# Optimization experiments

Hardware: AMD Instinct MI355X
Metric: run time of the kernel (lower is better)

## Reference

```python
import jax, jax.numpy as jnp
import numpy as np

SCALE = 8.0  # sqrt(head_dim=64); module divides scores by self.scale


def setup_inputs() -> dict:
    key = jax.random.key(0)
    kq, kk, kv = jax.random.split(key, 3)
    B, H, L, D = 4, 8, 2048, 64
    queries = jax.random.normal(kq, (B, H, L, D), dtype=jnp.float32)
    keys = jax.random.normal(kk, (B, H, L, D), dtype=jnp.float32)
    values = jax.random.normal(kv, (B, H, L, D), dtype=jnp.float32)
    return {"queries": queries, "keys": keys, "values": values}


def reference(queries, keys, values):
    # scores: [B, H, L_Q, L_K]
    L_Q, L_K = queries.shape[2], keys.shape[2]
    scores = jnp.einsum('bnqd,bnkd->bnqk', queries, keys) / SCALE
    # causal mask: triu(ones, diagonal=1) positions set to -inf
    causal = jnp.triu(jnp.ones((L_Q, L_K), dtype=bool), k=1)
    scores = jnp.where(causal[None, None, :, :], -jnp.inf, scores)
    A = jax.nn.softmax(scores, axis=-1)  # dropout p=0.0 (eval) -> identity
    V = jnp.einsum('bnqk,bnkd->bnqd', A, values)
    return V
```

## Files before the change

### kernel.cpp

```cpp
#include <hip/hip_runtime.h>
#include <hip/hip_bf16.h>

typedef __attribute__((ext_vector_type(8))) short bf16x8;
typedef __attribute__((ext_vector_type(16))) float f32x16;

#define DHEAD 64
#define L_SEQ 2048
#define QSCALE (0.125f * 1.44269504088896340736f)

#define WS_ML_OFF   4096
#define WS_PART_OFF (4096 + 512 * 2 * 128 * 8)
#define WS_NEED     ((size_t)WS_PART_OFF + (size_t)512 * 128 * 64 * 2)

union U4S8 { uint4 u; bf16x8 s; };

__device__ __forceinline__ unsigned pk2(float a, float b) {
    unsigned r;
    asm("v_cvt_pk_bf16_f32 %0, %1, %2" : "=v"(r) : "v"(a), "v"(b));
    return r;
}
__device__ __forceinline__ float bfrt(float x) {
    return __uint_as_float(pk2(x, x) << 16);
}
__device__ __forceinline__ float bf2f(unsigned short u) {
    return __uint_as_float((unsigned)u << 16);
}

__device__ __forceinline__ float fexp2(float x) {
#if __has_builtin(__builtin_amdgcn_exp2f)
    return __builtin_amdgcn_exp2f(x);
#else
    return __expf(x * 0.69314718055994530942f);
#endif
}

#if __has_builtin(__builtin_amdgcn_permlane32_swap)
__device__ __forceinline__ float xhalf_max(float x) {
    const unsigned u = __float_as_uint(x);
    const auto r = __builtin_amdgcn_permlane32_swap(u, u, false, false);
    return fmaxf(__uint_as_float(r[0]), __uint_as_float(r[1]));
}
__device__ __forceinline__ float xhalf_sum(float x) {
    const unsigned u = __float_as_uint(x);
    const auto r = __builtin_amdgcn_permlane32_swap(u, u, false, false);
    return __uint_as_float(r[0]) + __uint_as_float(r[1]);
}
#else
__device__ __forceinline__ float xhalf_max(float x) { return fmaxf(x, __shfl_xor(x, 32)); }
__device__ __forceinline__ float xhalf_sum(float x) { return x + __shfl_xor(x, 32); }
#endif

#define MAX16(P) fmaxf(fmaxf(fmaxf(fmaxf(P[0],P[1]),fmaxf(P[2],P[3])),          \
                             fmaxf(fmaxf(P[4],P[5]),fmaxf(P[6],P[7]))),         \
                       fmaxf(fmaxf(fmaxf(P[8],P[9]),fmaxf(P[10],P[11])),        \
                             fmaxf(fmaxf(P[12],P[13]),fmaxf(P[14],P[15]))))
#define SUM16(P) ((((P[0]+P[1])+(P[2]+P[3]))+((P[4]+P[5])+(P[6]+P[7])))         \
                + (((P[8]+P[9])+(P[10]+P[11]))+((P[12]+P[13])+(P[14]+P[15]))))


template<int SPLIT>
__global__ __launch_bounds__(256, 3)
void fattn_kernel(const float* __restrict__ Qg, const float* __restrict__ Kg,
                  const float* __restrict__ Vg, float* __restrict__ Og,
                  char* __restrict__ wsBase) {
    __shared__ uint4 sK4[16][64];
    __shared__ uint4 sV4[16][64];

    const int tid  = threadIdx.x;
    const int lane = tid & 63;
    const int w    = tid >> 6;
    const int hi   = lane >> 5;
    const int c    = lane & 31;

    const int id  = blockIdx.x;
    const int bh  = (id & 7) + 8 * ((id >> 3) & 3);

    int T, h, kt0, kstep, d;
    if (SPLIT) {
        const int k31 = 31 - (id >> 5);
        T = k31 >> 1;
        h = 1 - (k31 & 1);
        d = (T + 2 - h) >> 1;
        if (d == 0) return;
        kt0 = h; kstep = 2;
    } else {
        const int u_ = id >> 5;
        T = (u_ < 8) ? (15 - u_) : (u_ - 8);
        h = 0; d = T + 1; kt0 = 0; kstep = 1;
    }

    const size_t base = (size_t)bh * L_SEQ * DHEAD;
    const int q0w = T * 128 + w * 32;

    bf16x8 qf[4];
    {
        const float* Qrow = Qg + base + (size_t)(q0w + c) * DHEAD;
        #pragma unroll
        for (int kc = 0; kc < 4; ++kc) {
            float4 aa = *(const float4*)(Qrow + kc * 16 + hi * 8);
            float4 bb = *(const float4*)(Qrow + kc * 16 + hi * 8 + 4);
            U4S8 t;
            t.u = make_uint4(pk2(aa.x * QSCALE, aa.y * QSCALE),
                             pk2(aa.z * QSCALE, aa.w * QSCALE),
                             pk2(bb.x * QSCALE, bb.y * QSCALE),
                             pk2(bb.z * QSCALE, bb.w * QSCALE));
            qf[kc] = t.s;
        }
    }

    const float* Kpb = Kg + base + (size_t)(32 * w + c) * DHEAD + 32 * hi;
    const float* Vpb = Vg + base + (size_t)(32 * w + 16 * hi) * DHEAD + c;

    auto stage_K = [&](int kt) {
        float4 rk[8];
        const float* Kp = Kpb + (size_t)kt * 128 * DHEAD;
        #pragma unroll
        for (int t = 0; t < 8; ++t) rk[t] = *(const float4*)(Kp + 4 * t);
        #pragma unroll
        for (int q = 0; q < 2; ++q)
            #pragma unroll
            for (int hh = 0; hh < 2; ++hh) {
                const float4 r0 = rk[4 * q + 2 * hh], r1 = rk[4 * q + 2 * hh + 1];
                sK4[w * 4 + 2 * hi + q][hh * 32 + c] =
                    make_uint4(pk2(r0.x, r0.y), pk2(r0.z, r0.w),
                               pk2(r1.x, r1.y), pk2(r1.z, r1.w));
            }
    };
    auto stage_V = [&](int kt) {
        float rv[32];
        const float* Vp = Vpb + (size_t)kt * 128 * DHEAD;
        #pragma unroll
        for (int j = 0; j < 16; ++j) {
            rv[j]      = Vp[j * DHEAD];
            rv[16 + j] = Vp[j * DHEAD + 32];
        }
        #pragma unroll
        for (int dt = 0; dt < 2; ++dt)
            #pragma unroll
            for (int hh = 0; hh < 2; ++hh) {
                const int b = 16 * dt + 8 * hh;
                sV4[(2 * w + hi) * 2 + dt][hh * 32 + c] =
                    make_uint4(pk2(rv[b + 0], rv[b + 1]), pk2(rv[b + 2], rv[b + 3]),
                               pk2(rv[b + 4], rv[b + 5]), pk2(rv[b + 6], rv[b + 7]));
            }
    };

    f32x16 o0 = {0,0,0,0,0,0,0,0,0,0,0,0,0,0,0,0};
    f32x16 o1 = o0;
    float m_r = -1e30f, l_r = 0.f;

    stage_K(kt0);
    stage_V(kt0);
    __syncthreads();

    for (int j = 0; j < d; ++j) {
        const int  kt   = kt0 + j * kstep;
        const bool pf   = (j + 1 < d);
        const bool diag = (kt == T);

        #pragma unroll
        for (int sub = 0; sub < 2; ++sub) {
            const int lim = diag ? (w + 1 - 2 * sub) : 2;
            const int nkb = lim < 0 ? 0 : (lim > 2 ? 2 : lim);
            if (nkb > 0) {
                float p[2][16];

                __builtin_amdgcn_s_setprio(1);
                #pragma unroll
                for (int i = 0; i < 2; ++i) {
                    if (i < nkb) {
                        f32x16 s = {0,0,0,0,0,0,0,0,0,0,0,0,0,0,0,0};
                        #pragma unroll
                        for (int kc = 0; kc < 4; ++kc) {
                            U4S8 t; t.u = sK4[(2 * sub + i) * 4 + kc][lane];
                            s = __builtin_amdgcn_mfma_f32_32x32x16_bf16(t.s, qf[kc], s, 0, 0, 0);
                        }
                        #pragma unroll
                        for (int r = 0; r < 16; ++r) p[i][r] = s[r];
                    }
                }
                __builtin_amdgcn_s_setprio(0);

                #pragma unroll
                for (int i = 0; i < 2; ++i) {
                    if (diag && (2 * sub + i) == w) {
                        #pragma unroll
                        for (int r = 0; r < 16; ++r) {
                            const int kk = (r & 3) + 8 * (r >> 2) + 4 * hi;
                            if (kk > c) p[i][r] = -1e30f;
                        }
                    }
                }

                float mx = MAX16(p[0]);
                if (nkb > 1) mx = fmaxf(mx, MAX16(p[1]));
                mx = xhalf_max(mx);

                if (__any(mx > m_r + 8.f)) {
                    const float mn    = fmaxf(m_r, mx);
                    const float alpha = fexp2(m_r - mn);
                    m_r  = mn;
                    l_r *= alpha;
                    #pragma unroll
                    for (int r = 0; r < 16; ++r) {
                        const float ab = __shfl(alpha, (r & 3) + 8 * (r >> 2) + 4 * hi);
                        o0[r] *= ab; o1[r] *= ab;
                    }
                }

                #pragma unroll
                for (int i = 0; i < 2; ++i) {
                    if (i < nkb) {
                        #pragma unroll
                        for (int r = 0; r < 16; ++r) p[i][r] = fexp2(p[i][r] - m_r);
                    }
                }
                float rs = SUM16(p[0]);
                if (nkb > 1) rs += SUM16(p[1]);
                rs = xhalf_sum(rs);
                l_r += rs;

                __builtin_amdgcn_s_setprio(1);
                #pragma unroll
                for (int kcl = 0; kcl < 4; ++kcl) {
                    if (kcl < 2 * nkb) {
                        const int i = kcl >> 1, bs = (kcl & 1) * 8;
                        unsigned a0 = pk2(p[i][bs + 0], p[i][bs + 1]);
                        unsigned a1 = pk2(p[i][bs + 2], p[i][bs + 3]);
                        unsigned b0 = pk2(p[i][bs + 4], p[i][bs + 5]);
                        unsigned b1 = pk2(p[i][bs + 6], p[i][bs + 7]);
                        asm("v_permlane32_swap_b32 %0, %1" : "+v"(a0), "+v"(b0));
                        asm("v_permlane32_swap_b32 %0, %1" : "+v"(a1), "+v"(b1));
                        U4S8 t;
                        t.u = make_uint4(a0, a1, b0, b1);
                        const int kv = 4 * sub + kcl;
                        U4S8 tv0; tv0.u = sV4[kv * 2][lane];
                        o0 = __builtin_amdgcn_mfma_f32_32x32x16_bf16(t.s, tv0.s, o0, 0, 0, 0);
                        U4S8 tv1; tv1.u = sV4[kv * 2 + 1][lane];
                        o1 = __builtin_amdgcn_mfma_f32_32x32x16_bf16(t.s, tv1.s, o1, 0, 0, 0);
                    }
                }
                __builtin_amdgcn_s_setprio(0);
            }
        }

        if (pf) {
            __syncthreads();
            stage_K(kt + kstep);
            stage_V(kt + kstep);
            __syncthreads();
        }
    }

    float* Op = Og + base;

    if (!SPLIT || T == 0) {
        const float linv = 1.f / l_r;
        #pragma unroll
        for (int r = 0; r < 16; ++r) {
            const int   cr  = (r & 3) + 8 * (r >> 2) + 4 * hi;
            const float lb  = __shfl(linv, cr);
            const int   row = q0w + cr;
            Op[(size_t)row * DHEAD + c]      = o0[r] * lb;
            Op[(size_t)row * DHEAD + 32 + c] = o1[r] * lb;
        }
        return;
    }

    const int f = bh * 16 + T;
    float2* ml = (float2*)(wsBase + WS_ML_OFF);
    if (hi == 0) ml[((size_t)f * 2 + h) * 128 + w * 32 + c] = make_float2(m_r, l_r);
    if (h == 0) {
        #pragma unroll
        for (int r = 0; r < 16; ++r) {
            const int cr  = (r & 3) + 8 * (r >> 2) + 4 * hi;
            const int row = q0w + cr;
            Op[(size_t)row * DHEAD + c]      = bfrt(o0[r]);
            Op[(size_t)row * DHEAD + 32 + c] = bfrt(o1[r]);
        }
    } else {
        unsigned short* mp = (unsigned short*)(wsBase + WS_PART_OFF) + (size_t)f * 128 * 64;
        #pragma unroll
        for (int r = 0; r < 16; ++r) {
            const int cr   = (r & 3) + 8 * (r >> 2) + 4 * hi;
            const int lrow = w * 32 + cr;
            mp[lrow * 64 + c]      = (unsigned short)pk2(o0[r], o0[r]);
            mp[lrow * 64 + 32 + c] = (unsigned short)pk2(o1[r], o1[r]);
        }
    }
}

__global__ __launch_bounds__(256)
void merge_kernel(float* __restrict__ Og, const char* __restrict__ wsBase) {
    const int blk = blockIdx.x;
    const int bh = blk >> 4, T = blk & 15;
    if (T == 0) return;
    const int f = bh * 16 + T;

    const float2* ml = (const float2*)(wsBase + WS_ML_OFF);
    const unsigned short* part =
        (const unsigned short*)(wsBase + WS_PART_OFF) + (size_t)f * 128 * 64;
    float* Op = Og + ((size_t)bh * L_SEQ + (size_t)T * 128) * DHEAD;

    __shared__ float sA0[128], sA1[128], sLi[128];
    const int t = threadIdx.x;
    if (t < 128) {
        const float2 m0 = ml[((size_t)f * 2 + 0) * 128 + t];
        const float2 m1 = ml[((size_t)f * 2 + 1) * 128 + t];
        const float mM = fmaxf(m0.x, m1.x);
        const float a0 = fexp2(m0.x - mM);
        const float a1 = fexp2(m1.x - mM);
        sA0[t] = a0; sA1[t] = a1;
        sLi[t] = 1.f / (a0 * m0.y + a1 * m1.y);
    }
    __syncthreads();

    #pragma unroll
    for (int e = 0; e < 8; ++e) {
        const int idx4 = e * 256 + t;
        const int row  = idx4 >> 4;
        const int c4   = (idx4 & 15) * 4;
        const float a0 = sA0[row], a1 = sA1[row], li = sLi[row];
        float4 po = *(float4*)&Op[row * 64 + c4];
        const ushort4 u = *(const ushort4*)&part[row * 64 + c4];
        po.x = (a0 * po.x + a1 * bf2f(u.x)) * li;
        po.y = (a0 * po.y + a1 * bf2f(u.y)) * li;
        po.z = (a0 * po.z + a1 * bf2f(u.z)) * li;
        po.w = (a0 * po.w + a1 * bf2f(u.w)) * li;
        *(float4*)&Op[row * 64 + c4] = po;
    }
}

extern "C" void kernel_launch(void* const* d_in, const int* in_sizes, int n_in,
                              void* d_out, int out_size, void* d_ws, size_t ws_size,
                              hipStream_t stream) {
    const float* Q = (const float*)d_in[0];
    const float* K = (const float*)d_in[1];
    const float* V = (const float*)d_in[2];
    float* O = (float*)d_out;
    if (ws_size >= WS_NEED) {
        fattn_kernel<1><<<dim3(1024), dim3(256), 0, stream>>>(Q, K, V, O, (char*)d_ws);
        merge_kernel<<<dim3(512), dim3(256), 0, stream>>>(O, (const char*)d_ws);
    } else {
        fattn_kernel<0><<<dim3(512), dim3(256), 0, stream>>>(Q, K, V, O, (char*)d_ws);
    }
}
```

Measured before the change: 51.77 us.

## Pre-convert K to bf16 and V to transposed bf16 in separate prepass kernels

```diff
diff --git a/kernel.cpp b/kernel.cpp
--- a/kernel.cpp
+++ b/kernel.cpp
@@ -10,7 +10,10 @@
 
 #define WS_ML_OFF   4096
 #define WS_PART_OFF (4096 + 512 * 2 * 128 * 8)
-#define WS_NEED     ((size_t)WS_PART_OFF + (size_t)512 * 128 * 64 * 2)
+#define WS_KB_OFF   ((size_t)10 * 1024 * 1024)
+#define WS_VT_OFF   ((size_t)18 * 1024 * 1024)
+#define WS_NEED_B   ((size_t)WS_PART_OFF + (size_t)512 * 128 * 64 * 2)
+#define WS_NEED_A   ((size_t)26 * 1024 * 1024)
 
 union U4S8 { uint4 u; bf16x8 s; };
 
@@ -25,7 +28,6 @@
 __device__ __forceinline__ float bf2f(unsigned short u) {
     return __uint_as_float((unsigned)u << 16);
 }
-
 __device__ __forceinline__ float fexp2(float x) {
 #if __has_builtin(__builtin_amdgcn_exp2f)
     return __builtin_amdgcn_exp2f(x);
@@ -57,8 +59,43 @@
 #define SUM16(P) ((((P[0]+P[1])+(P[2]+P[3]))+((P[4]+P[5])+(P[6]+P[7])))         \
                 + (((P[8]+P[9])+(P[10]+P[11]))+((P[12]+P[13])+(P[14]+P[15]))))
 
-
-template<int SPLIT>
+__global__ __launch_bounds__(256)
+void conv_k(const float* __restrict__ K, unsigned short* __restrict__ Kb) {
+    const size_t i = ((size_t)blockIdx.x * 256 + threadIdx.x) * 8;
+    const float4 a = *(const float4*)(K + i);
+    const float4 b = *(const float4*)(K + i + 4);
+    *(uint4*)(Kb + i) = make_uint4(pk2(a.x, a.y), pk2(a.z, a.w),
+                                   pk2(b.x, b.y), pk2(b.z, b.w));
+}
+
+__global__ __launch_bounds__(256)
+void conv_vt(const float* __restrict__ V, unsigned short* __restrict__ Vt) {
+    __shared__ unsigned short lt[64][72];
+    const int bh = blockIdx.x >> 5, sb = blockIdx.x & 31;
+    const int t = threadIdx.x, r = t >> 2, c0 = (t & 3) * 16;
+    const float* Vp = V + ((size_t)bh * L_SEQ + sb * 64 + r) * DHEAD + c0;
+    const float4 a = ((const float4*)Vp)[0], b = ((const float4*)Vp)[1];
+    const float4 cc = ((const float4*)Vp)[2], d = ((const float4*)Vp)[3];
+    *(uint4*)&lt[r][c0]     = make_uint4(pk2(a.x, a.y), pk2(a.z, a.w),
+                                         pk2(b.x, b.y), pk2(b.z, b.w));
+    *(uint4*)&lt[r][c0 + 8] = make_uint4(pk2(cc.x, cc.y), pk2(cc.z, cc.w),
+                                         pk2(d.x, d.y), pk2(d.z, d.w));
+    __syncthreads();
+    const int dd = t >> 2, s0 = (t & 3) * 16;
+    unsigned short tmp[16];
+    #pragma unroll
+    for (int j = 0; j < 16; ++j) tmp[j] = lt[s0 + j][dd];
+    unsigned u[8];
+    #pragma unroll
+    for (int j = 0; j < 8; ++j)
+        u[j] = (unsigned)tmp[2 * j] | ((unsigned)tmp[2 * j + 1] << 16);
+    unsigned short* o = Vt + ((size_t)bh * 64 + dd) * L_SEQ + sb * 64 + s0;
+    ((uint4*)o)[0] = make_uint4(u[0], u[1], u[2], u[3]);
+    ((uint4*)o)[1] = make_uint4(u[4], u[5], u[6], u[7]);
+}
+
+
+template<int SPLIT, int PRE>
 __global__ __launch_bounds__(256, 3)
 void fattn_kernel(const float* __restrict__ Qg, const float* __restrict__ Kg,
                   const float* __restrict__ Vg, float* __restrict__ Og,
@@ -110,39 +147,69 @@
 
     const float* Kpb = Kg + base + (size_t)(32 * w + c) * DHEAD + 32 * hi;
     const float* Vpb = Vg + base + (size_t)(32 * w + 16 * hi) * DHEAD + c;
+    const unsigned short* KbB = (const unsigned short*)(wsBase + WS_KB_OFF)
+                              + base + (size_t)(32 * w + c) * DHEAD + 32 * hi;
+    const unsigned short* VtB = (const unsigned short*)(wsBase + WS_VT_OFF)
+                              + (size_t)bh * 64 * L_SEQ + (2 * w + hi) * 16;
 
     auto stage_K = [&](int kt) {
-        float4 rk[8];
-        const float* Kp = Kpb + (size_t)kt * 128 * DHEAD;
-        #pragma unroll
-        for (int t = 0; t < 8; ++t) rk[t] = *(const float4*)(Kp + 4 * t);
-        #pragma unroll
-        for (int q = 0; q < 2; ++q)
+        if (PRE) {
+            const unsigned short* Kt = KbB + (size_t)kt * 128 * DHEAD;
+            const uint4 k00 = *(const uint4*)(Kt + 0);
+            const uint4 k01 = *(const uint4*)(Kt + 8);
+            const uint4 k10 = *(const uint4*)(Kt + 16);
+            const uint4 k11 = *(const uint4*)(Kt + 24);
+            sK4[w * 4 + 2 * hi][c]          = k00;
+            sK4[w * 4 + 2 * hi][32 + c]     = k01;
+            sK4[w * 4 + 2 * hi + 1][c]      = k10;
+            sK4[w * 4 + 2 * hi + 1][32 + c] = k11;
+        } else {
+            float4 rk[8];
+            const float* Kp = Kpb + (size_t)kt * 128 * DHEAD;
             #pragma unroll
-            for (int hh = 0; hh < 2; ++hh) {
-                const float4 r0 = rk[4 * q + 2 * hh], r1 = rk[4 * q + 2 * hh + 1];
-                sK4[w * 4 + 2 * hi + q][hh * 32 + c] =
-                    make_uint4(pk2(r0.x, r0.y), pk2(r0.z, r0.w),
-                               pk2(r1.x, r1.y), pk2(r1.z, r1.w));
-            }
+            for (int t = 0; t < 8; ++t) rk[t] = *(const float4*)(Kp + 4 * t);
+            #pragma unroll
+            for (int q = 0; q < 2; ++q)
+                #pragma unroll
+                for (int hh = 0; hh < 2; ++hh) {
+                    const float4 r0 = rk[4 * q + 2 * hh], r1 = rk[4 * q + 2 * hh + 1];
+                    sK4[w * 4 + 2 * hi + q][hh * 32 + c] =
+                        make_uint4(pk2(r0.x, r0.y), pk2(r0.z, r0.w),
+                                   pk2(r1.x, r1.y), pk2(r1.z, r1.w));
+                }
+        }
     };
     auto stage_V = [&](int kt) {
-        float rv[32];
-        const float* Vp = Vpb + (size_t)kt * 128 * DHEAD;
-        #pragma unroll
-        for (int j = 0; j < 16; ++j) {
-            rv[j]      = Vp[j * DHEAD];
-            rv[16 + j] = Vp[j * DHEAD + 32];
-        }
-        #pragma unroll
-        for (int dt = 0; dt < 2; ++dt)
+        if (PRE) {
+            const unsigned short* Vk = VtB + (size_t)kt * 128;
+            const unsigned short* Vr0 = Vk + (size_t)c * L_SEQ;
+            const unsigned short* Vr1 = Vk + (size_t)(32 + c) * L_SEQ;
+            const uint4 v00 = *(const uint4*)(Vr0 + 0);
+            const uint4 v01 = *(const uint4*)(Vr0 + 8);
+            const uint4 v10 = *(const uint4*)(Vr1 + 0);
+            const uint4 v11 = *(const uint4*)(Vr1 + 8);
+            sV4[(2 * w + hi) * 2][c]          = v00;
+            sV4[(2 * w + hi) * 2][32 + c]     = v01;
+            sV4[(2 * w + hi) * 2 + 1][c]      = v10;
+            sV4[(2 * w + hi) * 2 + 1][32 + c] = v11;
+        } else {
+            float rv[32];
+            const float* Vp = Vpb + (size_t)kt * 128 * DHEAD;
             #pragma unroll
-            for (int hh = 0; hh < 2; ++hh) {
-                const int b = 16 * dt + 8 * hh;
-                sV4[(2 * w + hi) * 2 + dt][hh * 32 + c] =
-                    make_uint4(pk2(rv[b + 0], rv[b + 1]), pk2(rv[b + 2], rv[b + 3]),
-                               pk2(rv[b + 4], rv[b + 5]), pk2(rv[b + 6], rv[b + 7]));
+            for (int j = 0; j < 16; ++j) {
+                rv[j]      = Vp[j * DHEAD];
+                rv[16 + j] = Vp[j * DHEAD + 32];
             }
+            #pragma unroll
+            for (int dt = 0; dt < 2; ++dt)
+                #pragma unroll
+                for (int hh = 0; hh < 2; ++hh) {
+                    const int b = 16 * dt + 8 * hh;
+                    sV4[(2 * w + hi) * 2 + dt][hh * 32 + c] =
+                        make_uint4(pk2(rv[b + 0], rv[b + 1]), pk2(rv[b + 2], rv[b + 3]),
+                                   pk2(rv[b + 4], rv[b + 5]), pk2(rv[b + 6], rv[b + 7]));
+                }
+        }
     };
 
     f32x16 o0 = {0,0,0,0,0,0,0,0,0,0,0,0,0,0,0,0};
@@ -338,10 +405,16 @@
     const float* K = (const float*)d_in[1];
     const float* V = (const float*)d_in[2];
     float* O = (float*)d_out;
-    if (ws_size >= WS_NEED) {
-        fattn_kernel<1><<<dim3(1024), dim3(256), 0, stream>>>(Q, K, V, O, (char*)d_ws);
-        merge_kernel<<<dim3(512), dim3(256), 0, stream>>>(O, (const char*)d_ws);
+    char* ws = (char*)d_ws;
+    if (ws_size >= WS_NEED_A) {
+        conv_k<<<dim3(2048), dim3(256), 0, stream>>>(K, (unsigned short*)(ws + WS_KB_OFF));
+        conv_vt<<<dim3(1024), dim3(256), 0, stream>>>(V, (unsigned short*)(ws + WS_VT_OFF));
+        fattn_kernel<1, 1><<<dim3(1024), dim3(256), 0, stream>>>(Q, K, V, O, ws);
+        merge_kernel<<<dim3(512), dim3(256), 0, stream>>>(O, ws);
+    } else if (ws_size >= WS_NEED_B) {
+        fattn_kernel<1, 0><<<dim3(1024), dim3(256), 0, stream>>>(Q, K, V, O, ws);
+        merge_kernel<<<dim3(512), dim3(256), 0, stream>>>(O, ws);
     } else {
-        fattn_kernel<0><<<dim3(512), dim3(256), 0, stream>>>(Q, K, V, O, (char*)d_ws);
-    }
-}
+        fattn_kernel<0, 0><<<dim3(512), dim3(256), 0, stream>>>(Q, K, V, O, ws);
+    }
+}
```

New measurement: 57.50 us. 1.11x slower.
